# Kernel tuning notes

Hardware: AMD Instinct MI355X
Metric: run time of the kernel (lower is better)

The kernel has to match this reference:

```python
import jax, jax.numpy as jnp
import numpy as np

MAX_SEQ_LEN = 1000

def _ln(x, g, b, eps=1e-5):
    m = jnp.mean(x, -1, keepdims=True)
    v = jnp.var(x, -1, keepdims=True)
    return (x - m) * jax.lax.rsqrt(v + eps) * g + b

def _conv1d(x, k, b):
    # x [B,T,Cin], k [K,Cin,Cout], 'SAME' padding (odd kernel)
    return jax.lax.conv_general_dilated(x, k, (1,), 'SAME', dimension_numbers=('NWC', 'WIO', 'NWC')) + b

def _dwconv(x, w):
    # lightweight conv: softmax-normalized depthwise kernel, w [C,K]
    k = jnp.transpose(jax.nn.softmax(w, axis=1))[:, None, :]  # [K,1,C]
    return jax.lax.conv_general_dilated(x, k, (1,), 'SAME', dimension_numbers=('NWC', 'WIO', 'NWC'), feature_group_count=x.shape[-1])

def _conv2d(x, k, b):
    # x [B,H,W,Cin], k [kh,kw,Cin,Cout]
    return jax.lax.conv_general_dilated(x, k, (1, 1), 'SAME', dimension_numbers=('NHWC', 'HWIO', 'NHWC')) + b

def _lconv(x, mask, ln_g, ln_b, glu_w, glu_b, dw, out_w, out_b):
    # LConvBlock: LN -> GLU projection -> depthwise lightweight conv -> out proj -> residual, masked
    res = x
    h = _ln(x, ln_g, ln_b)
    h = h @ glu_w + glu_b
    a, g = jnp.split(h, 2, axis=-1)
    h = a * jax.nn.sigmoid(g)
    h = jnp.where(mask[..., None], 0.0, h)
    h = _dwconv(h, dw)
    h = h @ out_w + out_b
    h = h + res
    return jnp.where(mask[..., None], 0.0, h)

def _forward(content_embedding, speaker_embedding_B, rhythm_B, scaled_duration_outputs,
             in_w, in_b,
             lc0_ln_g, lc0_ln_b, lc0_glu_w, lc0_glu_b, lc0_dw, lc0_out_w, lc0_out_b,
             lc1_ln_g, lc1_ln_b, lc1_glu_w, lc1_glu_b, lc1_dw, lc1_out_w, lc1_out_b,
             p1_w, p1_b, p2_k, p2_b,
             cw_k, cw_b, cw_ln_g, cw_ln_b,
             mkb1_k, mkb1_b, mkb2_k, mkb2_b,
             lw_w, lw_b, ln_g, ln_b, text_mask):
    B, S, _ = content_embedding.shape
    spk = jnp.broadcast_to(speaker_embedding_B[:, None, :], (B, S, speaker_embedding_B.shape[-1]))
    x = jnp.concatenate([content_embedding, spk], -1) @ in_w + in_b
    # duration predictor
    V = _lconv(x, text_mask, lc0_ln_g, lc0_ln_b, lc0_glu_w, lc0_glu_b, lc0_dw, lc0_out_w, lc0_out_b)
    V = _lconv(V, text_mask, lc1_ln_g, lc1_ln_b, lc1_glu_w, lc1_glu_b, lc1_dw, lc1_out_w, lc1_out_b)
    D = jax.nn.softplus(V @ p1_w + p1_b)[..., 0]
    D = jnp.where(text_mask, 0.0, D)
    T = _conv1d(V, p2_k, p2_b)  # [B,S,upsampled_dim]
    # learnable upsampling
    pred_phoneme_len = scaled_duration_outputs.sum(-1)
    alpha_B = jax.lax.stop_gradient(pred_phoneme_len / rhythm_B) / D.sum(-1)
    sD = alpha_B[:, None] * D
    sV = alpha_B[:, None, None] * V
    sT = alpha_B[:, None, None] * T
    mel_len = jnp.clip(jnp.round(sD.sum(-1)).astype(jnp.int32), 1, MAX_SEQ_LEN)
    mel_mask = jnp.arange(MAX_SEQ_LEN)[None, :] >= mel_len[:, None]  # True = pad
    attn_mask = mel_mask[:, :, None] & text_mask[:, None, :]  # bmm(mel_mask, src_mask^T).bool()
    e_k = jnp.cumsum(sD, axis=1)
    s_k = e_k - sD
    t = jnp.arange(1, MAX_SEQ_LEN + 1, dtype=sD.dtype)[None, :, None]
    Sm = jnp.where(attn_mask, 0.0, t - s_k[:, None, :])
    Em = jnp.where(attn_mask, 0.0, e_k[:, None, :] - t)
    # conv_w block: conv1d -> relu -> LN
    Cv = _ln(jax.nn.relu(_conv1d(sV, cw_k, cw_b)), cw_ln_g, cw_ln_b)  # [B,S,CW]
    feat = jnp.concatenate([Sm[..., None], Em[..., None],
                            jnp.broadcast_to(Cv[:, None, :, :], (B, MAX_SEQ_LEN, S, Cv.shape[-1]))], -1)
    h = jax.nn.silu(_conv2d(feat, mkb1_k, mkb1_b))
    h = jax.nn.silu(_conv2d(h, mkb2_k, mkb2_b))
    Wsc = (h @ lw_w + lw_b)[..., 0]  # [B,mel,S]
    Wsc = jnp.where(attn_mask | text_mask[:, None, :], -jnp.inf, Wsc)
    Wmat = jax.nn.softmax(Wsc, axis=2)
    up = jnp.matmul(Wmat, sT)
    up = _ln(up, ln_g, ln_b)
    up = jnp.where(mel_mask[..., None], 0.0, up)
    return up, Wmat, alpha_B, mel_len, mel_mask

def setup_inputs() -> dict:
    key = jax.random.key(0)
    ks = iter(jax.random.split(key, 64))
    B, S, DC, DS, H, CW, MKB, K = 8, 256, 192, 64, 256, 16, 16, 3
    def w(shape, scale=0.02):
        return jax.random.normal(next(ks), shape, jnp.float32) * scale
    inp = {}
    inp['content_embedding'] = jax.random.normal(next(ks), (B, S, DC), jnp.float32)
    inp['speaker_embedding_B'] = jax.random.normal(next(ks), (B, DS), jnp.float32)
    inp['rhythm_B'] = 0.15 + 0.1 * jax.random.uniform(next(ks), (B,), jnp.float32)
    inp['scaled_duration_outputs'] = jax.random.uniform(next(ks), (B, S), jnp.float32)
    lens = jax.random.randint(next(ks), (B,), 200, S + 1)
    inp['text_mask'] = jnp.arange(S)[None, :] >= lens[:, None]
    inp['in_w'] = w((DC + DS, H)); inp['in_b'] = jnp.zeros((H,), jnp.float32)
    for i in range(2):
        inp[f'lc{i}_ln_g'] = jnp.ones((H,), jnp.float32); inp[f'lc{i}_ln_b'] = jnp.zeros((H,), jnp.float32)
        inp[f'lc{i}_glu_w'] = w((H, 2 * H)); inp[f'lc{i}_glu_b'] = jnp.zeros((2 * H,), jnp.float32)
        inp[f'lc{i}_dw'] = w((H, K), 1.0)
        inp[f'lc{i}_out_w'] = w((H, H)); inp[f'lc{i}_out_b'] = jnp.zeros((H,), jnp.float32)
    inp['p1_w'] = w((H, 1)); inp['p1_b'] = jnp.zeros((1,), jnp.float32)
    inp['p2_k'] = w((K, H, H)); inp['p2_b'] = jnp.zeros((H,), jnp.float32)
    inp['cw_k'] = w((K, H, CW)); inp['cw_b'] = jnp.zeros((CW,), jnp.float32)
    inp['cw_ln_g'] = jnp.ones((CW,), jnp.float32); inp['cw_ln_b'] = jnp.zeros((CW,), jnp.float32)
    inp['mkb1_k'] = w((K, K, CW + 2, MKB)); inp['mkb1_b'] = jnp.zeros((MKB,), jnp.float32)
    inp['mkb2_k'] = w((K, K, MKB, MKB)); inp['mkb2_b'] = jnp.zeros((MKB,), jnp.float32)
    inp['lw_w'] = w((MKB, 1)); inp['lw_b'] = jnp.zeros((1,), jnp.float32)
    inp['ln_g'] = jnp.ones((H,), jnp.float32); inp['ln_b'] = jnp.zeros((H,), jnp.float32)
    return inp

def reference(content_embedding, speaker_embedding_B, rhythm_B, scaled_duration_outputs,
              text_mask,
              in_w, in_b,
              lc0_ln_g, lc0_ln_b, lc0_glu_w, lc0_glu_b, lc0_dw, lc0_out_w, lc0_out_b,
              lc1_ln_g, lc1_ln_b, lc1_glu_w, lc1_glu_b, lc1_dw, lc1_out_w, lc1_out_b,
              p1_w, p1_b, p2_k, p2_b,
              cw_k, cw_b, cw_ln_g, cw_ln_b,
              mkb1_k, mkb1_b, mkb2_k, mkb2_b,
              lw_w, lw_b, ln_g, ln_b):
    return _forward(content_embedding, speaker_embedding_B, rhythm_B, scaled_duration_outputs,
                    in_w, in_b,
                    lc0_ln_g, lc0_ln_b, lc0_glu_w, lc0_glu_b, lc0_dw, lc0_out_w, lc0_out_b,
                    lc1_ln_g, lc1_ln_b, lc1_glu_w, lc1_glu_b, lc1_dw, lc1_out_w, lc1_out_b,
                    p1_w, p1_b, p2_k, p2_b,
                    cw_k, cw_b, cw_ln_g, cw_ln_b,
                    mkb1_k, mkb1_b, mkb2_k, mkb2_b,
                    lw_w, lw_b, ln_g, ln_b, text_mask)
```

## Files before the change

### kernel.cpp

```cpp
#include <hip/hip_runtime.h>
#include <math.h>

#define SS 256
#define HH 256
#define MLEN 1000
#define CWW 16
#define NOC 16
#define RB 24

typedef __attribute__((ext_vector_type(8))) short bfrag;
typedef __attribute__((ext_vector_type(4))) float ffrag;

#define WS_V2     1048576u
#define WS_STT    1835008u
#define WS_WB     2097152u
#define WS_CCV    2424832u
#define WS_SSV    2457600u
#define WS_CCI    2490368u
#define WS_SSI    2523136u
#define WS_CP     2555904u
#define WS_CV     2654208u
#define WS_EK     2686976u
#define WS_SK     2689024u
#define WS_ALPHA  2691072u
#define WS_MELI   2691080u
#define WS_TMASK  2691088u

#define PK_IN     0u
#define PK_GLU0   65536u
#define PK_GLU1   196608u
#define PK_OUT0   327680u
#define PK_OUT1   393216u
#define PK_P2     458752u

#define OUT_UP    0u
#define OUT_W     2048000u
#define OUT_ALPHA 4096000u
#define OUT_MLEN  4096008u
#define OUT_MMASK 4096016u

__device__ __forceinline__ unsigned bf16rne(float x){
  unsigned u=__float_as_uint(x);
  u += 0x7fffu + ((u>>16)&1u);
  return u;
}
__device__ __forceinline__ unsigned short bf16h(float x){ return (unsigned short)(bf16rne(x)>>16); }
__device__ __forceinline__ float bf2f(unsigned short u){ return __uint_as_float(((unsigned)u)<<16); }
__device__ __forceinline__ unsigned frag_idx(int k,int n,int KT){
  return (unsigned)(((((n>>4)*KT+(k>>5))*64 + ((k>>3)&3)*16 + (n&15))<<3) + (k&7));
}

__global__ __launch_bounds__(256) void k_prepmask(const void* __restrict__ traw,
    const float* __restrict__ in_w,
    const float* __restrict__ g0, const float* __restrict__ g1,
    const float* __restrict__ o0, const float* __restrict__ o1,
    const float* __restrict__ p2k, float* __restrict__ ws){
  int tid=threadIdx.x;
  if(blockIdx.x==256){
    __shared__ int s_fu, s_ff, s_nz;
    const unsigned char* mb=(const unsigned char*)traw;
    const unsigned int*  mw=(const unsigned int*)traw;
    if(tid==0){s_fu=0;s_ff=0;s_nz=0;}
    __syncthreads();
    int fu=0,ff=0,nz=0;
    for(int w=tid;w<512;w+=256){
      unsigned int v=mw[w];
      if(v){ nz=1; if(v==0x3F800000u) ff=1; else if(v&0xFFFFFF00u) fu=1; }
    }
    if(fu) atomicOr(&s_fu,1);
    if(ff) atomicOr(&s_ff,1);
    if(nz) atomicOr(&s_nz,1);
    __syncthreads();
    int words = (s_ff || (!s_fu && s_nz));
    for(int i=tid;i<2048;i+=256){
      unsigned int v = words ? mw[i] : (unsigned int)mb[i];
      ws[WS_TMASK+i] = v ? 1.0f : 0.0f;
    }
    return;
  }
  unsigned short* wb=(unsigned short*)(ws+WS_WB);
  int gid=blockIdx.x*256+tid, stride=65536;
  for(int i=gid;i<65536;i+=stride){ int k=i>>8,n=i&255; wb[PK_IN  +frag_idx(k,n,8)]=bf16h(in_w[i]); }
  for(int i=gid;i<131072;i+=stride){ int k=i>>9,n=i&511; wb[PK_GLU0+frag_idx(k,n,8)]=bf16h(g0[i]); }
  for(int i=gid;i<131072;i+=stride){ int k=i>>9,n=i&511; wb[PK_GLU1+frag_idx(k,n,8)]=bf16h(g1[i]); }
  for(int i=gid;i<65536;i+=stride){ int k=i>>8,n=i&255; wb[PK_OUT0+frag_idx(k,n,8)]=bf16h(o0[i]); }
  for(int i=gid;i<65536;i+=stride){ int k=i>>8,n=i&255; wb[PK_OUT1+frag_idx(k,n,8)]=bf16h(o1[i]); }
  for(int i=gid;i<196608;i+=stride){ int k3=i>>16,r=i&65535,k=r>>8,n=r&255;
    wb[PK_P2+(unsigned)k3*65536u+frag_idx(k,n,8)]=bf16h(p2k[i]); }
}

__global__ __launch_bounds__(256) void k_front(
    const float* __restrict__ ce, const float* __restrict__ spk,
    const unsigned short* __restrict__ wb, const float* __restrict__ in_b,
    const float* __restrict__ g0b, const float* __restrict__ ln0g, const float* __restrict__ ln0b,
    const float* __restrict__ dw0, const float* __restrict__ o0b,
    const float* __restrict__ g1b, const float* __restrict__ ln1g, const float* __restrict__ ln1b,
    const float* __restrict__ dw1, const float* __restrict__ o1b,
    const float* __restrict__ tmask, float* __restrict__ V2){
  __shared__ unsigned short Abf[16][264];
  __shared__ unsigned short Hb[16][264];
  __shared__ float Xf[16][264];
  __shared__ float Vf[16][264];
  __shared__ float dws[2][3][256];
  __shared__ float tmL[20];
  int b=blockIdx.x>>5, tile=blockIdx.x&31, s0=tile*8, tid=threadIdx.x;
  int w=tid>>6, lane=tid&63, lq=lane>>4, lm=lane&15;
  {
    float d0=dw0[tid*3],d1=dw0[tid*3+1],d2=dw0[tid*3+2];
    float mx=fmaxf(d0,fmaxf(d1,d2));
    float e0=__expf(d0-mx),e1=__expf(d1-mx),e2=__expf(d2-mx);
    float inv=1.0f/(e0+e1+e2);
    dws[0][0][tid]=e0*inv; dws[0][1][tid]=e1*inv; dws[0][2][tid]=e2*inv;
    d0=dw1[tid*3];d1=dw1[tid*3+1];d2=dw1[tid*3+2];
    mx=fmaxf(d0,fmaxf(d1,d2));
    e0=__expf(d0-mx);e1=__expf(d1-mx);e2=__expf(d2-mx);
    inv=1.0f/(e0+e1+e2);
    dws[1][0][tid]=e0*inv; dws[1][1][tid]=e1*inv; dws[1][2][tid]=e2*inv;
  }
  if(tid<18){
    int sI=s0-2+tid;
    tmL[tid]=(sI>=0&&sI<256)? tmask[b*256+sI] : 1.0f;
  }
  for(int it=0;it<16;it++){
    float v=0.f;
    int sI=s0-2+it;
    if(it<12 && sI>=0 && sI<256){
      int m=b*256+sI;
      v=(tid<192)? ce[m*192+tid] : spk[b*64+tid-192];
    }
    Abf[it][tid]=bf16h(v);
  }
  __syncthreads();
  {
    ffrag acc[4];
    #pragma unroll
    for(int j=0;j<4;j++){acc[j][0]=0;acc[j][1]=0;acc[j][2]=0;acc[j][3]=0;}
    #pragma unroll
    for(int kt=0;kt<8;kt++){
      bfrag af=*(const bfrag*)&Abf[lm][kt*32+lq*8];
      #pragma unroll
      for(int j=0;j<4;j++){
        int nt=w*4+j;
        bfrag bf=*(const bfrag*)(wb+PK_IN+((((unsigned)(nt*8+kt))*64u+(unsigned)lane)<<3));
        acc[j]=__builtin_amdgcn_mfma_f32_16x16x32_bf16(af,bf,acc[j],0,0,0);
      }
    }
    #pragma unroll
    for(int j=0;j<4;j++){
      int n=w*64+j*16+lm;
      float bn=in_b[n];
      #pragma unroll
      for(int reg=0;reg<4;reg++) Xf[lq*4+reg][n]=acc[j][reg]+bn;
    }
  }
  __syncthreads();
  {
    int r=tid>>4, seg=tid&15;
    if(r<12){
      float s=0.f,q=0.f;
      #pragma unroll
      for(int j4=0;j4<4;j4++){
        float4 v=*(const float4*)&Xf[r][seg*16+j4*4];
        s+=v.x+v.y+v.z+v.w; q+=v.x*v.x+v.y*v.y+v.z*v.z+v.w*v.w;
      }
      s+=__shfl_xor(s,1); q+=__shfl_xor(q,1);
      s+=__shfl_xor(s,2); q+=__shfl_xor(q,2);
      s+=__shfl_xor(s,4); q+=__shfl_xor(q,4);
      s+=__shfl_xor(s,8); q+=__shfl_xor(q,8);
      float mean=s*(1.0f/256.0f), rstd=rsqrtf(q*(1.0f/256.0f)-mean*mean+1e-5f);
      #pragma unroll
      for(int j4=0;j4<4;j4++){
        int c=seg*16+j4*4;
        float4 v=*(const float4*)&Xf[r][c];
        unsigned short q0=bf16h((v.x-mean)*rstd*ln0g[c+0]+ln0b[c+0]);
        unsigned short q1=bf16h((v.y-mean)*rstd*ln0g[c+1]+ln0b[c+1]);
        unsigned short q2=bf16h((v.z-mean)*rstd*ln0g[c+2]+ln0b[c+2]);
        unsigned short q3=bf16h((v.w-mean)*rstd*ln0g[c+3]+ln0b[c+3]);
        *(uint2*)&Abf[r][c]=make_uint2((unsigned)q0|((unsigned)q1<<16),(unsigned)q2|((unsigned)q3<<16));
      }
    } else {
      #pragma unroll
      for(int j4=0;j4<4;j4++) *(uint2*)&Abf[r][seg*16+j4*4]=make_uint2(0,0);
    }
  }
  __syncthreads();
  {
    ffrag aa[4],ag[4];
    #pragma unroll
    for(int j=0;j<4;j++){aa[j][0]=0;aa[j][1]=0;aa[j][2]=0;aa[j][3]=0;
                         ag[j][0]=0;ag[j][1]=0;ag[j][2]=0;ag[j][3]=0;}
    #pragma unroll
    for(int kt=0;kt<8;kt++){
      bfrag af=*(const bfrag*)&Abf[lm][kt*32+lq*8];
      #pragma unroll
      for(int j=0;j<4;j++){
        int nta=w*4+j, ntg=nta+16;
        bfrag bfa=*(const bfrag*)(wb+PK_GLU0+((((unsigned)(nta*8+kt))*64u+(unsigned)lane)<<3));
        bfrag bfg=*(const bfrag*)(wb+PK_GLU0+((((unsigned)(ntg*8+kt))*64u+(unsigned)lane)<<3));
        aa[j]=__builtin_amdgcn_mfma_f32_16x16x32_bf16(af,bfa,aa[j],0,0,0);
        ag[j]=__builtin_amdgcn_mfma_f32_16x16x32_bf16(af,bfg,ag[j],0,0,0);
      }
    }
    __syncthreads();
    #pragma unroll
    for(int j=0;j<4;j++){
      int n=w*64+j*16+lm;
      float ba=g0b[n], bg=g0b[n+256];
      #pragma unroll
      for(int reg=0;reg<4;reg++){
        int row=lq*4+reg;
        float a=aa[j][reg]+ba, g=ag[j][reg]+bg;
        float hv=a*(1.0f/(1.0f+__expf(-g)));
        if(row>=12||tmL[row]!=0.0f) hv=0.0f;
        Hb[row][n]=bf16h(hv);
      }
    }
  }
  __syncthreads();
  {
    float w0=dws[0][0][tid],w1=dws[0][1][tid],w2=dws[0][2][tid];
    for(int r=0;r<10;r++){
      float a=w0*bf2f(Hb[r][tid])+w1*bf2f(Hb[r+1][tid])+w2*bf2f(Hb[r+2][tid]);
      Abf[r][tid]=bf16h(a);
    }
    for(int r=10;r<16;r++) Abf[r][tid]=0;
  }
  __syncthreads();
  {
    ffrag acc[4];
    #pragma unroll
    for(int j=0;j<4;j++){acc[j][0]=0;acc[j][1]=0;acc[j][2]=0;acc[j][3]=0;}
    #pragma unroll
    for(int kt=0;kt<8;kt++){
      bfrag af=*(const bfrag*)&Abf[lm][kt*32+lq*8];
      #pragma unroll
      for(int j=0;j<4;j++){
        int nt=w*4+j;
        bfrag bf=*(const bfrag*)(wb+PK_OUT0+((((unsigned)(nt*8+kt))*64u+(unsigned)lane)<<3));
        acc[j]=__builtin_amdgcn_mfma_f32_16x16x32_bf16(af,bf,acc[j],0,0,0);
      }
    }
    #pragma unroll
    for(int j=0;j<4;j++){
      int n=w*64+j*16+lm;
      float bn=o0b[n];
      #pragma unroll
      for(int reg=0;reg<4;reg++){
        int row=lq*4+reg;
        float v=(row<10 && tmL[row+1]==0.0f)? acc[j][reg]+bn+Xf[row+1][n] : 0.0f;
        Vf[row][n]=v;
      }
    }
  }
  __syncthreads();
  {
    int r=tid>>4, seg=tid&15;
    if(r<10){
      float s=0.f,q=0.f;
      #pragma unroll
      for(int j4=0;j4<4;j4++){
        float4 v=*(const float4*)&Vf[r][seg*16+j4*4];
        s+=v.x+v.y+v.z+v.w; q+=v.x*v.x+v.y*v.y+v.z*v.z+v.w*v.w;
      }
      s+=__shfl_xor(s,1); q+=__shfl_xor(q,1);
      s+=__shfl_xor(s,2); q+=__shfl_xor(q,2);
      s+=__shfl_xor(s,4); q+=__shfl_xor(q,4);
      s+=__shfl_xor(s,8); q+=__shfl_xor(q,8);
      float mean=s*(1.0f/256.0f), rstd=rsqrtf(q*(1.0f/256.0f)-mean*mean+1e-5f);
      #pragma unroll
      for(int j4=0;j4<4;j4++){
        int c=seg*16+j4*4;
        float4 v=*(const float4*)&Vf[r][c];
        unsigned short q0=bf16h((v.x-mean)*rstd*ln1g[c+0]+ln1b[c+0]);
        unsigned short q1=bf16h((v.y-mean)*rstd*ln1g[c+1]+ln1b[c+1]);
        unsigned short q2=bf16h((v.z-mean)*rstd*ln1g[c+2]+ln1b[c+2]);
        unsigned short q3=bf16h((v.w-mean)*rstd*ln1g[c+3]+ln1b[c+3]);
        *(uint2*)&Abf[r][c]=make_uint2((unsigned)q0|((unsigned)q1<<16),(unsigned)q2|((unsigned)q3<<16));
      }
    } else {
      #pragma unroll
      for(int j4=0;j4<4;j4++) *(uint2*)&Abf[r][seg*16+j4*4]=make_uint2(0,0);
    }
  }
  __syncthreads();
  {
    ffrag aa[4],ag[4];
    #pragma unroll
    for(int j=0;j<4;j++){aa[j][0]=0;aa[j][1]=0;aa[j][2]=0;aa[j][3]=0;
                         ag[j][0]=0;ag[j][1]=0;ag[j][2]=0;ag[j][3]=0;}
    #pragma unroll
    for(int kt=0;kt<8;kt++){
      bfrag af=*(const bfrag*)&Abf[lm][kt*32+lq*8];
      #pragma unroll
      for(int j=0;j<4;j++){
        int nta=w*4+j, ntg=nta+16;
        bfrag bfa=*(const bfrag*)(wb+PK_GLU1+((((unsigned)(nta*8+kt))*64u+(unsigned)lane)<<3));
        bfrag bfg=*(const bfrag*)(wb+PK_GLU1+((((unsigned)(ntg*8+kt))*64u+(unsigned)lane)<<3));
        aa[j]=__builtin_amdgcn_mfma_f32_16x16x32_bf16(af,bfa,aa[j],0,0,0);
        ag[j]=__builtin_amdgcn_mfma_f32_16x16x32_bf16(af,bfg,ag[j],0,0,0);
      }
    }
    __syncthreads();
    #pragma unroll
    for(int j=0;j<4;j++){
      int n=w*64+j*16+lm;
      float ba=g1b[n], bg=g1b[n+256];
      #pragma unroll
      for(int reg=0;reg<4;reg++){
        int row=lq*4+reg;
        float a=aa[j][reg]+ba, g=ag[j][reg]+bg;
        float hv=a*(1.0f/(1.0f+__expf(-g)));
        if(row>=10||tmL[row+1]!=0.0f) hv=0.0f;
        Hb[row][n]=bf16h(hv);
      }
    }
  }
  __syncthreads();
  {
    float w0=dws[1][0][tid],w1=dws[1][1][tid],w2=dws[1][2][tid];
    for(int r=0;r<8;r++){
      float a=w0*bf2f(Hb[r][tid])+w1*bf2f(Hb[r+1][tid])+w2*bf2f(Hb[r+2][tid]);
      Abf[r][tid]=bf16h(a);
    }
    for(int r=8;r<16;r++) Abf[r][tid]=0;
  }
  __syncthreads();
  {
    ffrag acc[4];
    #pragma unroll
    for(int j=0;j<4;j++){acc[j][0]=0;acc[j][1]=0;acc[j][2]=0;acc[j][3]=0;}
    #pragma unroll
    for(int kt=0;kt<8;kt++){
      bfrag af=*(const bfrag*)&Abf[lm][kt*32+lq*8];
      #pragma unroll
      for(int j=0;j<4;j++){
        int nt=w*4+j;
        bfrag bf=*(const bfrag*)(wb+PK_OUT1+((((unsigned)(nt*8+kt))*64u+(unsigned)lane)<<3));
        acc[j]=__builtin_amdgcn_mfma_f32_16x16x32_bf16(af,bf,acc[j],0,0,0);
      }
    }
    #pragma unroll
    for(int j=0;j<4;j++){
      int n=w*64+j*16+lm;
      float bn=o1b[n];
      #pragma unroll
      for(int reg=0;reg<4;reg++){
        int row=lq*4+reg;
        if(row<8){
          float v=(tmL[row+2]!=0.0f)? 0.0f : acc[j][reg]+bn+Vf[row+1][n];
          V2[(unsigned)(b*256+s0+row)*256u+n]=v;
        }
      }
    }
  }
}

__global__ __launch_bounds__(256) void k_dur(const float* __restrict__ V2, const float* __restrict__ p1w,
    const float* __restrict__ p1b, const float* __restrict__ sdo, const float* __restrict__ rhythm,
    float* __restrict__ ws, float* __restrict__ outp){
  __shared__ float p1[HH];
  __shared__ float sd[SS];
  __shared__ float red[16];
  int b=blockIdx.x, tid=threadIdx.x;
  int wid=tid>>6, lane=tid&63;
  p1[tid]=p1w[tid];
  __syncthreads();
  float accd=p1b[0];
  const float* row=V2+(unsigned)(b*SS+tid)*HH;
  for(int k=0;k<HH;k+=4){
    float4 v=*(const float4*)&row[k];
    accd+=v.x*p1[k]+v.y*p1[k+1]+v.z*p1[k+2]+v.w*p1[k+3];
  }
  float Dv=fmaxf(accd,0.0f)+log1pf(expf(-fabsf(accd)));
  if(ws[WS_TMASK+b*SS+tid]!=0.0f) Dv=0.0f;
  float sv=sdo[b*SS+tid];
  float a=Dv, c=sv;
  for(int off=32;off;off>>=1){ a+=__shfl_down(a,off); c+=__shfl_down(c,off); }
  if(lane==0){ red[wid]=a; red[wid+8]=c; }
  __syncthreads();
  float Dsum=red[0]+red[1]+red[2]+red[3];
  float pred=red[8]+red[9]+red[10]+red[11];
  float al=(pred/rhythm[b])/Dsum;
  float sDv=al*Dv;
  sd[tid]=sDv;
  __syncthreads();
  for(int off=1;off<SS;off<<=1){
    float t=(tid>=off)?sd[tid-off]:0.0f;
    __syncthreads();
    sd[tid]+=t;
    __syncthreads();
  }
  float ek=sd[tid], sk=ek-sDv;
  ws[WS_EK+b*SS+tid]=ek;
  ws[WS_SK+b*SS+tid]=sk;
  float melf=sd[SS-1];
  int mel=(int)rintf(melf); mel=mel<1?1:(mel>MLEN?MLEN:mel);
  if(tid==0){
    ws[WS_ALPHA+b]=al;
    ((int*)ws)[WS_MELI+b]=mel;
    outp[OUT_ALPHA+b]=al;
    outp[OUT_MLEN+b]=(float)mel;
  }
  for(int t=tid;t<MLEN;t+=SS) outp[OUT_MMASK+b*MLEN+t]=(t>=mel)?1.0f:0.0f;
}

__global__ __launch_bounds__(256) void k_post(const float* __restrict__ V2,
    const unsigned short* __restrict__ wbp2, const float* __restrict__ p2b,
    const float* __restrict__ cwk, const float* __restrict__ cwb,
    const float* __restrict__ cwg, const float* __restrict__ cwbe,
    const float* __restrict__ mkb1k, const float* __restrict__ mkb1b,
    float* __restrict__ ws){
  int bx=blockIdx.x, tid=threadIdx.x;
  if(bx<256){
    __shared__ unsigned short Abf[18][264];
    int m0=(bx>>1)*16, nh=bx&1, b=m0>>8, s0=m0&255;
    for(int it=0;it<18;it++){
      int sI=s0-1+it;
      float v=(sI>=0&&sI<256)? V2[(unsigned)(b*256+sI)*256u+tid] : 0.0f;
      Abf[it][tid]=bf16h(v);
    }
    __syncthreads();
    int w=tid>>6, lane=tid&63, lq=lane>>4, lm=lane&15;
    ffrag acc[2];
    #pragma unroll
    for(int tt=0;tt<2;tt++){ acc[tt][0]=0;acc[tt][1]=0;acc[tt][2]=0;acc[tt][3]=0; }
    for(int k3=0;k3<3;k3++){
      const unsigned short* wb3=wbp2+(unsigned)k3*65536u;
      #pragma unroll
      for(int kt=0;kt<8;kt++){
        bfrag af=*(const bfrag*)&Abf[lm+k3][kt*32+lq*8];
        #pragma unroll
        for(int tt=0;tt<2;tt++){
          int nt=nh*8+w*2+tt;
          bfrag bf=*(const bfrag*)(wb3+((((unsigned)(nt*8+kt))*64u+(unsigned)lane)<<3));
          acc[tt]=__builtin_amdgcn_mfma_f32_16x16x32_bf16(af,bf,acc[tt],0,0,0);
        }
      }
    }
    float al=ws[WS_ALPHA+b];
    unsigned short* stt=(unsigned short*)(ws+WS_STT);
    #pragma unroll
    for(int tt=0;tt<2;tt++){
      int n=nh*128+w*32+tt*16+lm;
      float bn=p2b[n];
      unsigned short o0=bf16h((acc[tt][0]+bn)*al);
      unsigned short o1=bf16h((acc[tt][1]+bn)*al);
      unsigned short o2=bf16h((acc[tt][2]+bn)*al);
      unsigned short o3=bf16h((acc[tt][3]+bn)*al);
      *(uint2*)&stt[((unsigned)(b*256+n)<<8)+(unsigned)(s0+lq*4)]=
        make_uint2((unsigned)o0|((unsigned)o1<<16),(unsigned)o2|((unsigned)o3<<16));
    }
  } else if(bx<384){
    __shared__ float Vt[18][SS];
    int bb=bx-256;
    int b=bb>>4, tile=bb&15;
    int sbase=tile*16;
    float al=ws[WS_ALPHA+b];
    for(int rr=0;rr<18;rr++){
      int s=sbase-1+rr;
      Vt[rr][tid]=(s>=0&&s<SS)?al*V2[(b*SS+s)*HH+tid]:0.0f;
    }
    __syncthreads();
    int sl=tid>>4, oc=tid&15;
    float a0=cwb[oc],a1=0.f,a2=0.f,a3=0.f;
    for(int k3=0;k3<3;k3++){
      const float* vp=&Vt[sl+k3][0];
      const float* wpp=cwk+(unsigned)k3*HH*CWW+oc;
      for(int c=0;c<HH;c+=4){
        a0+=vp[c+0]*wpp[(c+0)*CWW];
        a1+=vp[c+1]*wpp[(c+1)*CWW];
        a2+=vp[c+2]*wpp[(c+2)*CWW];
        a3+=vp[c+3]*wpp[(c+3)*CWW];
      }
    }
    float acc=fmaxf((a0+a1)+(a2+a3),0.0f);
    float ssum=acc, qsum=acc*acc;
    for(int off=8;off;off>>=1){ ssum+=__shfl_xor(ssum,off); qsum+=__shfl_xor(qsum,off); }
    float mean=ssum*(1.0f/CWW), var=qsum*(1.0f/CWW)-mean*mean;
    float cv=(acc-mean)*rsqrtf(var+1e-5f)*cwg[oc]+cwbe[oc];
    ws[WS_CV+(unsigned)(b*SS+sbase+sl)*CWW+oc]=cv;
  } else {
    __shared__ float CvL[258][17];
    __shared__ float k1c[3][3][CWW][NOC];
    __shared__ float kab[3][3][2][NOC];
    __shared__ float skE[258], ekE[258], fiE[258];
    int b=bx-384;
    for(int i=tid;i<3*3*CWW*NOC;i+=256){
      int oc=i&15, ic=(i>>4)&15, kk=i>>8;
      int kw=kk%3, kh=kk/3;
      k1c[kh][kw][ic][oc]=mkb1k[((kh*3+kw)*18+2+ic)*NOC+oc];
    }
    for(int i=tid;i<3*3*2*NOC;i+=256){
      int oc=i&15, ch=(i>>4)&1, kk=i>>5;
      int kw=kk%3, kh=kk/3;
      kab[kh][kw][ch][oc]=mkb1k[((kh*3+kw)*18+ch)*NOC+oc];
    }
    for(int i=tid;i<SS*CWW;i+=256) CvL[1+(i>>4)][i&15]=ws[WS_CV+(unsigned)b*SS*CWW+i];
    if(tid<CWW){ CvL[0][tid]=0.f; CvL[257][tid]=0.f; }
    if(tid<258){
      float sk=0.f, ek=0.f, fi=0.f;
      if(tid>=1 && tid<=SS){
        sk=ws[WS_SK+b*SS+tid-1];
        ek=ws[WS_EK+b*SS+tid-1];
        fi=(ws[WS_TMASK+b*SS+tid-1]!=0.0f)?0.0f:1.0f;
      }
      skE[tid]=sk; ekE[tid]=ek; fiE[tid]=fi;
    }
    __syncthreads();
    float* cpg=ws+WS_CP+(unsigned)b*3*SS*NOC;
    float ccv[16],ssv[16],cci[16],ssi[16];
    #pragma unroll
    for(int oc=0;oc<NOC;oc++){ float bb2=mkb1b[oc]; ccv[oc]=bb2; cci[oc]=bb2; ssv[oc]=0.f; ssi[oc]=0.f; }
    for(int dt=0;dt<3;dt++){
      float acc[NOC];
      #pragma unroll
      for(int oc=0;oc<NOC;oc++) acc[oc]=0.f;
      #pragma unroll
      for(int ds=0;ds<3;ds++){
        #pragma unroll
        for(int ic=0;ic<CWW;ic++){
          float v=CvL[tid+ds][ic];
          #pragma unroll
          for(int oc=0;oc<NOC;oc++) acc[oc]+=v*k1c[dt][ds][ic][oc];
        }
      }
      for(int oc=0;oc<NOC;oc++) cpg[(unsigned)(dt*SS+tid)*NOC+oc]=acc[oc];
      float va[16],vb[16],ia[16],ib2[16];
      #pragma unroll
      for(int oc=0;oc<NOC;oc++){ va[oc]=0.f; vb[oc]=0.f; ia[oc]=0.f; ib2[oc]=0.f; }
      #pragma unroll
      for(int ds=0;ds<3;ds++){
        int j=tid+ds;
        float inb=(j>=1&&j<=SS)?1.0f:0.0f;
        float fb=fiE[j];
        float skv=skE[j], ekv=ekE[j];
        #pragma unroll
        for(int oc=0;oc<NOC;oc++){
          float ka=kab[dt][ds][0][oc], kb=kab[dt][ds][1][oc];
          float d=ka-kb, e=kb*ekv-ka*skv;
          va[oc]+=inb*d; vb[oc]+=inb*e; ia[oc]+=fb*d; ib2[oc]+=fb*e;
        }
      }
      float dtf=(float)dt;
      #pragma unroll
      for(int oc=0;oc<NOC;oc++){
        ccv[oc]+=acc[oc]+vb[oc]+dtf*va[oc]; ssv[oc]+=va[oc];
        cci[oc]+=acc[oc]+ib2[oc]+dtf*ia[oc]; ssi[oc]+=ia[oc];
      }
    }
    unsigned base=(unsigned)(b*SS+tid)*16u;
    for(int oc=0;oc<NOC;oc++){
      ws[WS_CCV+base+oc]=ccv[oc];
      ws[WS_SSV+base+oc]=ssv[oc];
      ws[WS_CCI+base+oc]=cci[oc];
      ws[WS_SSI+base+oc]=ssi[oc];
    }
  }
}

__global__ __launch_bounds__(256,4) void k_stageB(
    const float* __restrict__ ws, const float* __restrict__ mkb1k, const float* __restrict__ mkb1b,
    const float* __restrict__ mkb2k, const float* __restrict__ mkb2b,
    const float* __restrict__ lww, const float* __restrict__ lwb,
    float* __restrict__ outp){
  __shared__ short ringh[3][258][RB];
  __shared__ float skL[258], ekL[258];
  __shared__ unsigned char finC[260];
  __shared__ __align__(16) float wscL[SS];
  __shared__ float red[16];
  int bx=blockIdx.x, b=bx/125, chunk=bx%125, t0=chunk*8, tid=threadIdx.x;
  int wid=tid>>6, lane=tid&63;
  int lq=lane>>4, lm=lane&15;
  if(tid<258){
    float sk=0.f, ek=0.f; unsigned char fin=0;
    if(tid>=1 && tid<=SS){
      sk=ws[WS_SK+b*SS+tid-1];
      ek=ws[WS_EK+b*SS+tid-1];
      fin=(ws[WS_TMASK+b*SS+tid-1]!=0.0f)?0:1;
    }
    skL[tid]=sk; ekL[tid]=ek; finC[tid]=fin;
  }
  if(tid<72){
    int sl=tid/24, rem=tid%24;
    int row=(rem<12)?0:257, c=(rem%12)*2;
    *(int*)&ringh[sl][row][c]=0;
  }
  int mel=((const int*)ws)[WS_MELI+b];
  __syncthreads();

  const float* cpb=ws+WS_CP+(unsigned)b*3*SS*NOC;

  unsigned offA[5]; int dtL[5], zgL[5];
  bfrag bfw[5];
  {
    #pragma unroll
    for(int i=0;i<5;i++){
      int g=4*i+lq;
      int dt,ds,hf,zg;
      if(g<18){ dt=g/6; int rm=g-6*dt; ds=rm>>1; hf=rm&1; zg=0; }
      else { dt=0; ds=0; hf=0; zg=1; }
      int srow=wid*64+lm+ds;
      offA[i]=(unsigned)((srow*RB+8*hf)*2);
      dtL[i]=dt; zgL[i]=zg;
      int pk[4];
      if(!zg){
        #pragma unroll
        for(int j=0;j<4;j++){
          unsigned u0=bf16rne(mkb2k[(8*g+2*j)*NOC+lm]);
          unsigned u1=bf16rne(mkb2k[(8*g+2*j+1)*NOC+lm]);
          pk[j]=(int)((u0>>16)|(u1&0xffff0000u));
        }
      } else pk[0]=pk[1]=pk[2]=pk[3]=0;
      bfw[i]=__builtin_bit_cast(bfrag, make_int4(pk[0],pk[1],pk[2],pk[3]));
    }
  }
  float b2v=mkb2b[lm];
  float lwwv=lww[lm];
  float lwb0=lwb[0];
  const char* ringB=(const char*)&ringh[0][0][0];
  bfrag azero={};

  auto conv1row=[&](int T){
    int s=tid;
    float acc[NOC];
    bool fv=(T>=1)&&(T<=998)&&(T+1<mel);
    bool fi=(T>=2)&&(T<=998)&&(T-1>=mel);
    if(fv||fi){
      const float* cc=ws+(fv?WS_CCV:WS_CCI)+(unsigned)(b*SS+s)*16u;
      const float* s2=ws+(fv?WS_SSV:WS_SSI)+(unsigned)(b*SS+s)*16u;
      float Tf=(float)T;
      #pragma unroll
      for(int q=0;q<4;q++){
        float4 c4=((const float4*)cc)[q];
        float4 s4=((const float4*)s2)[q];
        acc[4*q+0]=c4.x+Tf*s4.x; acc[4*q+1]=c4.y+Tf*s4.y;
        acc[4*q+2]=c4.z+Tf*s4.z; acc[4*q+3]=c4.w+Tf*s4.w;
      }
    } else {
      #pragma unroll
      for(int oc=0;oc<NOC;oc++) acc[oc]=mkb1b[oc];
      #pragma unroll
      for(int dt=0;dt<3;dt++){
        int tr=T+dt-1;
        if(tr<0||tr>=MLEN) continue;
        bool valid=(tr<mel);
        float tt=(float)(tr+1);
        float gg[3], hh[3];
        #pragma unroll
        for(int ds=0;ds<3;ds++){
          int j=s+ds;
          float f = valid ? ((j>=1&&j<=SS)?1.0f:0.0f) : (float)finC[j];
          gg[ds]=f*(tt-skL[j]);
          hh[ds]=f*(ekL[j]-tt);
        }
        const float* cpr=cpb+(unsigned)(dt*SS+s)*NOC;
        float4 c0=((const float4*)cpr)[0], c1=((const float4*)cpr)[1];
        float4 c2=((const float4*)cpr)[2], c3=((const float4*)cpr)[3];
        acc[0]+=c0.x; acc[1]+=c0.y; acc[2]+=c0.z; acc[3]+=c0.w;
        acc[4]+=c1.x; acc[5]+=c1.y; acc[6]+=c1.z; acc[7]+=c1.w;
        acc[8]+=c2.x; acc[9]+=c2.y; acc[10]+=c2.z; acc[11]+=c2.w;
        acc[12]+=c3.x; acc[13]+=c3.y; acc[14]+=c3.z; acc[15]+=c3.w;
        #pragma unroll
        for(int ds=0;ds<3;ds++){
          const float* kA=mkb1k+((dt*3+ds)*18+0)*NOC;
          const float* kB=mkb1k+((dt*3+ds)*18+1)*NOC;
          #pragma unroll
          for(int oc=0;oc<NOC;oc++) acc[oc]+=gg[ds]*kA[oc]+hh[ds]*kB[oc];
        }
      }
    }
    int slot=T%3;
    int pk[8];
    #pragma unroll
    for(int j=0;j<8;j++){
      float x0=acc[2*j], x1=acc[2*j+1];
      float s0=x0/(1.0f+__expf(-x0));
      float s1=x1/(1.0f+__expf(-x1));
      unsigned u0=bf16rne(s0), u1=bf16rne(s1);
      pk[j]=(int)((u0>>16)|(u1&0xffff0000u));
    }
    int4* dst=(int4*)&ringh[slot][s+1][0];
    dst[0]=make_int4(pk[0],pk[1],pk[2],pk[3]);
    dst[1]=make_int4(pk[4],pk[5],pk[6],pk[7]);
  };

  if(t0>0) conv1row(t0-1);
  conv1row(t0);

  #pragma unroll 1
  for(int r=0;r<8;r++){
    int t=t0+r;
    if(t+1<MLEN) conv1row(t+1);
    __syncthreads();
    int tmod=t%3;
    ffrag acc2[4];
    #pragma unroll
    for(int tt=0;tt<4;tt++){ acc2[tt][0]=b2v; acc2[tt][1]=b2v; acc2[tt][2]=b2v; acc2[tt][3]=b2v; }
    #pragma unroll
    for(int i=0;i<5;i++){
      int dt=dtL[i];
      int x=tmod+dt+2; x=(x>=3)?x-3:x; x=(x>=3)?x-3:x;
      int tr=t+dt-1;
      bool av=((unsigned)tr<(unsigned)MLEN)&&(!zgL[i]);
      const char* rp=ringB+(unsigned)x*(258u*RB*2u)+offA[i];
      #pragma unroll
      for(int tt=0;tt<4;tt++){
        int4 ra=*(const int4*)(rp+tt*(16*RB*2));
        bfrag a=av?__builtin_bit_cast(bfrag,ra):azero;
        acc2[tt]=__builtin_amdgcn_mfma_f32_16x16x32_bf16(a,bfw[i],acc2[tt],0,0,0);
      }
    }
    #pragma unroll
    for(int tt=0;tt<4;tt++){
      float out4[4];
      #pragma unroll
      for(int q=0;q<4;q++){
        float xx=acc2[tt][q];
        float pv=(xx/(1.0f+__expf(-xx)))*lwwv;
        pv+=__shfl_xor(pv,1); pv+=__shfl_xor(pv,2); pv+=__shfl_xor(pv,4); pv+=__shfl_xor(pv,8);
        out4[q]=pv+lwb0;
      }
      if(lm==0){
        *(float4*)&wscL[wid*64+tt*16+lq*4]=make_float4(out4[0],out4[1],out4[2],out4[3]);
      }
    }
    __syncthreads();
    float fm=(float)finC[tid+1];
    float wsc=wscL[tid];
    float val=(fm!=0.0f)?wsc:-3.0e38f;
    float mx=val;
    for(int off=32;off;off>>=1) mx=fmaxf(mx,__shfl_down(mx,off));
    if(lane==0) red[wid]=mx;
    __syncthreads();
    mx=fmaxf(fmaxf(red[0],red[1]),fmaxf(red[2],red[3]));
    float e=(fm!=0.0f)?__expf(wsc-mx):0.0f;
    float sm=e;
    for(int off=32;off;off>>=1) sm+=__shfl_down(sm,off);
    if(lane==0) red[8+wid]=sm;
    __syncthreads();
    sm=red[8]+red[9]+red[10]+red[11];
    outp[OUT_W+(unsigned)(b*MLEN+t)*SS+tid]=e/sm;
    __syncthreads();
  }
}

__global__ __launch_bounds__(256) void k_up(const float* __restrict__ ws,
    const float* __restrict__ lng, const float* __restrict__ lnb, float* __restrict__ outp){
  __shared__ unsigned short Wbf[16][264];
  __shared__ float UpL[16][264];
  __shared__ float gb[2][256];
  int bx=blockIdx.x, b=bx/63, tile=bx%63, t0=tile*16, tid=threadIdx.x;
  gb[0][tid]=lng[tid]; gb[1][tid]=lnb[tid];
  for(int it=0;it<16;it++){
    int t=t0+it;
    float v=(t<MLEN)? outp[OUT_W+(unsigned)(b*MLEN+t)*256u+tid] : 0.0f;
    Wbf[it][tid]=bf16h(v);
  }
  int mel=((const int*)ws)[WS_MELI+b];
  __syncthreads();
  int w=tid>>6, lane=tid&63, lq=lane>>4, lm=lane&15;
  const unsigned short* stt=(const unsigned short*)(ws+WS_STT)+(unsigned)b*65536u;
  ffrag acc[4];
  #pragma unroll
  for(int tt=0;tt<4;tt++){ acc[tt][0]=0;acc[tt][1]=0;acc[tt][2]=0;acc[tt][3]=0; }
  #pragma unroll
  for(int kt=0;kt<8;kt++){
    bfrag af=*(const bfrag*)&Wbf[lm][kt*32+lq*8];
    #pragma unroll
    for(int tt=0;tt<4;tt++){
      int n=w*64+tt*16+lm;
      bfrag bf=*(const bfrag*)(stt+((unsigned)n<<8)+(unsigned)(kt*32+lq*8));
      acc[tt]=__builtin_amdgcn_mfma_f32_16x16x32_bf16(af,bf,acc[tt],0,0,0);
    }
  }
  #pragma unroll
  for(int tt=0;tt<4;tt++){
    #pragma unroll
    for(int reg=0;reg<4;reg++)
      UpL[lq*4+reg][w*64+tt*16+lm]=acc[tt][reg];
  }
  __syncthreads();
  int r=tid>>4, seg=tid&15;
  float s=0.f,q=0.f;
  #pragma unroll
  for(int j4=0;j4<4;j4++){
    float4 v=*(const float4*)&UpL[r][seg*16+j4*4];
    s+=v.x+v.y+v.z+v.w; q+=v.x*v.x+v.y*v.y+v.z*v.z+v.w*v.w;
  }
  s+=__shfl_xor(s,1); q+=__shfl_xor(q,1);
  s+=__shfl_xor(s,2); q+=__shfl_xor(q,2);
  s+=__shfl_xor(s,4); q+=__shfl_xor(q,4);
  s+=__shfl_xor(s,8); q+=__shfl_xor(q,8);
  float mean=s*(1.0f/256.0f), rstd=rsqrtf(q*(1.0f/256.0f)-mean*mean+1e-5f);
  int t=t0+r;
  if(t<MLEN){
    bool vld=(t<mel);
    #pragma unroll
    for(int j4=0;j4<4;j4++){
      int c=seg*16+j4*4;
      float4 v=*(const float4*)&UpL[r][c];
      float4 o;
      o.x=vld?((v.x-mean)*rstd*gb[0][c+0]+gb[1][c+0]):0.0f;
      o.y=vld?((v.y-mean)*rstd*gb[0][c+1]+gb[1][c+1]):0.0f;
      o.z=vld?((v.z-mean)*rstd*gb[0][c+2]+gb[1][c+2]):0.0f;
      o.w=vld?((v.w-mean)*rstd*gb[0][c+3]+gb[1][c+3]):0.0f;
      *(float4*)&outp[OUT_UP+(unsigned)(b*MLEN+t)*256u+c]=o;
    }
  }
}

extern "C" void kernel_launch(void* const* d_in, const int* in_sizes, int n_in,
                              void* d_out, int out_size, void* d_ws, size_t ws_size,
                              hipStream_t stream){
  const float* ce   =(const float*)d_in[0];
  const float* spk  =(const float*)d_in[1];
  const float* rhy  =(const float*)d_in[2];
  const float* sdo  =(const float*)d_in[3];
  const void*  tmr  =d_in[4];
  const float* in_w =(const float*)d_in[5];
  const float* in_b =(const float*)d_in[6];
  const float* l0lg =(const float*)d_in[7];
  const float* l0lb =(const float*)d_in[8];
  const float* l0gw =(const float*)d_in[9];
  const float* l0gb =(const float*)d_in[10];
  const float* l0dw =(const float*)d_in[11];
  const float* l0ow =(const float*)d_in[12];
  const float* l0ob =(const float*)d_in[13];
  const float* l1lg =(const float*)d_in[14];
  const float* l1lb =(const float*)d_in[15];
  const float* l1gw =(const float*)d_in[16];
  const float* l1gb =(const float*)d_in[17];
  const float* l1dw =(const float*)d_in[18];
  const float* l1ow =(const float*)d_in[19];
  const float* l1ob =(const float*)d_in[20];
  const float* p1w  =(const float*)d_in[21];
  const float* p1b  =(const float*)d_in[22];
  const float* p2k  =(const float*)d_in[23];
  const float* p2b  =(const float*)d_in[24];
  const float* cwk  =(const float*)d_in[25];
  const float* cwb  =(const float*)d_in[26];
  const float* cwg  =(const float*)d_in[27];
  const float* cwbe =(const float*)d_in[28];
  const float* m1k  =(const float*)d_in[29];
  const float* m1b  =(const float*)d_in[30];
  const float* m2k  =(const float*)d_in[31];
  const float* m2b  =(const float*)d_in[32];
  const float* lww  =(const float*)d_in[33];
  const float* lwbp =(const float*)d_in[34];
  const float* lng  =(const float*)d_in[35];
  const float* lnb  =(const float*)d_in[36];
  float* ws=(float*)d_ws;
  float* outp=(float*)d_out;
  const unsigned short* wbb=(const unsigned short*)(ws+WS_WB);

  k_prepmask<<<257,256,0,stream>>>(tmr, in_w, l0gw, l1gw, l0ow, l1ow, p2k, ws);
  k_front   <<<256,256,0,stream>>>(ce, spk, wbb, in_b,
                                   l0gb, l0lg, l0lb, l0dw, l0ob,
                                   l1gb, l1lg, l1lb, l1dw, l1ob,
                                   ws+WS_TMASK, ws+WS_V2);
  k_dur     <<<8,256,0,stream>>>(ws+WS_V2, p1w, p1b, sdo, rhy, ws, outp);
  k_post    <<<392,256,0,stream>>>(ws+WS_V2, wbb+PK_P2, p2b, cwk, cwb, cwg, cwbe, m1k, m1b, ws);
  k_stageB  <<<1000,256,0,stream>>>(ws, m1k, m1b, m2k, m2b, lww, lwbp, outp);
  k_up      <<<504,256,0,stream>>>(ws, lng, lnb, outp);
}
```

Baseline: 310.6 us.

## Halve k_front row tile to double block count; split cp stage into own kernel

k_front now handles 4 output rows per block instead of 8 and launches 512 blocks instead of 256. The goal is better fill of the GPU's compute units for this short front-end chain. The cost is more redundant halo rows per output, and the 16-row MFMA tiles are now mostly padding. The cp/mkb1 precompute branch moves out of k_post into its own 8-block kernel, which runs after the conv-LN blocks that write WS_CV. This removes the same-launch dependency but adds one more kernel launch.

```diff
diff --git a/kernel.cpp b/kernel.cpp
--- a/kernel.cpp
+++ b/kernel.cpp
@@ -98,12 +98,12 @@
     const float* __restrict__ dw1, const float* __restrict__ o1b,
     const float* __restrict__ tmask, float* __restrict__ V2){
   __shared__ unsigned short Abf[16][264];
-  __shared__ unsigned short Hb[16][264];
-  __shared__ float Xf[16][264];
-  __shared__ float Vf[16][264];
+  __shared__ unsigned short Hb[8][264];
+  __shared__ float Xf[8][264];
+  __shared__ float Vf[8][264];
   __shared__ float dws[2][3][256];
-  __shared__ float tmL[20];
-  int b=blockIdx.x>>5, tile=blockIdx.x&31, s0=tile*8, tid=threadIdx.x;
+  __shared__ float tmL[8];
+  int b=blockIdx.x>>6, tile=blockIdx.x&63, s0=tile*4, tid=threadIdx.x;
   int w=tid>>6, lane=tid&63, lq=lane>>4, lm=lane&15;
   {
     float d0=dw0[tid*3],d1=dw0[tid*3+1],d2=dw0[tid*3+2];
@@ -117,19 +117,20 @@
     inv=1.0f/(e0+e1+e2);
     dws[1][0][tid]=e0*inv; dws[1][1][tid]=e1*inv; dws[1][2][tid]=e2*inv;
   }
-  if(tid<18){
+  if(tid<8){
     int sI=s0-2+tid;
     tmL[tid]=(sI>=0&&sI<256)? tmask[b*256+sI] : 1.0f;
   }
-  for(int it=0;it<16;it++){
+  for(int it=0;it<8;it++){
     float v=0.f;
     int sI=s0-2+it;
-    if(it<12 && sI>=0 && sI<256){
+    if(sI>=0 && sI<256){
       int m=b*256+sI;
       v=(tid<192)? ce[m*192+tid] : spk[b*64+tid-192];
     }
     Abf[it][tid]=bf16h(v);
   }
+  for(int it=8;it<16;it++) Abf[it][tid]=0;
   __syncthreads();
   {
     ffrag acc[4];
@@ -150,13 +151,16 @@
       int n=w*64+j*16+lm;
       float bn=in_b[n];
       #pragma unroll
-      for(int reg=0;reg<4;reg++) Xf[lq*4+reg][n]=acc[j][reg]+bn;
+      for(int reg=0;reg<4;reg++){
+        int row=lq*4+reg;
+        if(row<8) Xf[row][n]=acc[j][reg]+bn;
+      }
     }
   }
   __syncthreads();
   {
     int r=tid>>4, seg=tid&15;
-    if(r<12){
+    if(r<8){
       float s=0.f,q=0.f;
       #pragma unroll
       for(int j4=0;j4<4;j4++){
@@ -178,9 +182,6 @@
         unsigned short q3=bf16h((v.w-mean)*rstd*ln0g[c+3]+ln0b[c+3]);
         *(uint2*)&Abf[r][c]=make_uint2((unsigned)q0|((unsigned)q1<<16),(unsigned)q2|((unsigned)q3<<16));
       }
-    } else {
-      #pragma unroll
-      for(int j4=0;j4<4;j4++) *(uint2*)&Abf[r][seg*16+j4*4]=make_uint2(0,0);
     }
   }
   __syncthreads();
@@ -209,21 +210,23 @@
       #pragma unroll
       for(int reg=0;reg<4;reg++){
         int row=lq*4+reg;
-        float a=aa[j][reg]+ba, g=ag[j][reg]+bg;
-        float hv=a*(1.0f/(1.0f+__expf(-g)));
-        if(row>=12||tmL[row]!=0.0f) hv=0.0f;
-        Hb[row][n]=bf16h(hv);
+        if(row<8){
+          float a=aa[j][reg]+ba, g=ag[j][reg]+bg;
+          float hv=a*(1.0f/(1.0f+__expf(-g)));
+          if(tmL[row]!=0.0f) hv=0.0f;
+          Hb[row][n]=bf16h(hv);
+        }
       }
     }
   }
   __syncthreads();
   {
     float w0=dws[0][0][tid],w1=dws[0][1][tid],w2=dws[0][2][tid];
-    for(int r=0;r<10;r++){
+    for(int r=0;r<6;r++){
       float a=w0*bf2f(Hb[r][tid])+w1*bf2f(Hb[r+1][tid])+w2*bf2f(Hb[r+2][tid]);
       Abf[r][tid]=bf16h(a);
     }
-    for(int r=10;r<16;r++) Abf[r][tid]=0;
+    Abf[6][tid]=0; Abf[7][tid]=0;
   }
   __syncthreads();
   {
@@ -247,15 +250,17 @@
       #pragma unroll
       for(int reg=0;reg<4;reg++){
         int row=lq*4+reg;
-        float v=(row<10 && tmL[row+1]==0.0f)? acc[j][reg]+bn+Xf[row+1][n] : 0.0f;
-        Vf[row][n]=v;
+        if(row<6){
+          float v=(tmL[row+1]==0.0f)? acc[j][reg]+bn+Xf[row+1][n] : 0.0f;
+          Vf[row][n]=v;
+        }
       }
     }
   }
   __syncthreads();
   {
     int r=tid>>4, seg=tid&15;
-    if(r<10){
+    if(r<6){
       float s=0.f,q=0.f;
       #pragma unroll
       for(int j4=0;j4<4;j4++){
@@ -277,9 +282,6 @@
         unsigned short q3=bf16h((v.w-mean)*rstd*ln1g[c+3]+ln1b[c+3]);
         *(uint2*)&Abf[r][c]=make_uint2((unsigned)q0|((unsigned)q1<<16),(unsigned)q2|((unsigned)q3<<16));
       }
-    } else {
-      #pragma unroll
-      for(int j4=0;j4<4;j4++) *(uint2*)&Abf[r][seg*16+j4*4]=make_uint2(0,0);
     }
   }
   __syncthreads();
@@ -308,21 +310,23 @@
       #pragma unroll
       for(int reg=0;reg<4;reg++){
         int row=lq*4+reg;
-        float a=aa[j][reg]+ba, g=ag[j][reg]+bg;
-        float hv=a*(1.0f/(1.0f+__expf(-g)));
-        if(row>=10||tmL[row+1]!=0.0f) hv=0.0f;
-        Hb[row][n]=bf16h(hv);
+        if(row<6){
+          float a=aa[j][reg]+ba, g=ag[j][reg]+bg;
+          float hv=a*(1.0f/(1.0f+__expf(-g)));
+          if(tmL[row+1]!=0.0f) hv=0.0f;
+          Hb[row][n]=bf16h(hv);
+        }
       }
     }
   }
   __syncthreads();
   {
     float w0=dws[1][0][tid],w1=dws[1][1][tid],w2=dws[1][2][tid];
-    for(int r=0;r<8;r++){
+    for(int r=0;r<4;r++){
       float a=w0*bf2f(Hb[r][tid])+w1*bf2f(Hb[r+1][tid])+w2*bf2f(Hb[r+2][tid]);
       Abf[r][tid]=bf16h(a);
     }
-    for(int r=8;r<16;r++) Abf[r][tid]=0;
+    Abf[4][tid]=0; Abf[5][tid]=0;
   }
   __syncthreads();
   {
@@ -346,7 +350,7 @@
       #pragma unroll
       for(int reg=0;reg<4;reg++){
         int row=lq*4+reg;
-        if(row<8){
+        if(row<4){
           float v=(tmL[row+2]!=0.0f)? 0.0f : acc[j][reg]+bn+Vf[row+1][n];
           V2[(unsigned)(b*256+s0+row)*256u+n]=v;
         }
@@ -408,7 +412,6 @@
     const unsigned short* __restrict__ wbp2, const float* __restrict__ p2b,
     const float* __restrict__ cwk, const float* __restrict__ cwb,
     const float* __restrict__ cwg, const float* __restrict__ cwbe,
-    const float* __restrict__ mkb1k, const float* __restrict__ mkb1b,
     float* __restrict__ ws){
   int bx=blockIdx.x, tid=threadIdx.x;
   if(bx<256){
@@ -450,7 +453,7 @@
       *(uint2*)&stt[((unsigned)(b*256+n)<<8)+(unsigned)(s0+lq*4)]=
         make_uint2((unsigned)o0|((unsigned)o1<<16),(unsigned)o2|((unsigned)o3<<16));
     }
-  } else if(bx<384){
+  } else {
     __shared__ float Vt[18][SS];
     int bb=bx-256;
     int b=bb>>4, tile=bb&15;
@@ -479,82 +482,85 @@
     float mean=ssum*(1.0f/CWW), var=qsum*(1.0f/CWW)-mean*mean;
     float cv=(acc-mean)*rsqrtf(var+1e-5f)*cwg[oc]+cwbe[oc];
     ws[WS_CV+(unsigned)(b*SS+sbase+sl)*CWW+oc]=cv;
-  } else {
-    __shared__ float CvL[258][17];
-    __shared__ float k1c[3][3][CWW][NOC];
-    __shared__ float kab[3][3][2][NOC];
-    __shared__ float skE[258], ekE[258], fiE[258];
-    int b=bx-384;
-    for(int i=tid;i<3*3*CWW*NOC;i+=256){
-      int oc=i&15, ic=(i>>4)&15, kk=i>>8;
-      int kw=kk%3, kh=kk/3;
-      k1c[kh][kw][ic][oc]=mkb1k[((kh*3+kw)*18+2+ic)*NOC+oc];
-    }
-    for(int i=tid;i<3*3*2*NOC;i+=256){
-      int oc=i&15, ch=(i>>4)&1, kk=i>>5;
-      int kw=kk%3, kh=kk/3;
-      kab[kh][kw][ch][oc]=mkb1k[((kh*3+kw)*18+ch)*NOC+oc];
-    }
-    for(int i=tid;i<SS*CWW;i+=256) CvL[1+(i>>4)][i&15]=ws[WS_CV+(unsigned)b*SS*CWW+i];
-    if(tid<CWW){ CvL[0][tid]=0.f; CvL[257][tid]=0.f; }
-    if(tid<258){
-      float sk=0.f, ek=0.f, fi=0.f;
-      if(tid>=1 && tid<=SS){
-        sk=ws[WS_SK+b*SS+tid-1];
-        ek=ws[WS_EK+b*SS+tid-1];
-        fi=(ws[WS_TMASK+b*SS+tid-1]!=0.0f)?0.0f:1.0f;
-      }
-      skE[tid]=sk; ekE[tid]=ek; fiE[tid]=fi;
-    }
-    __syncthreads();
-    float* cpg=ws+WS_CP+(unsigned)b*3*SS*NOC;
-    float ccv[16],ssv[16],cci[16],ssi[16];
-    #pragma unroll
-    for(int oc=0;oc<NOC;oc++){ float bb2=mkb1b[oc]; ccv[oc]=bb2; cci[oc]=bb2; ssv[oc]=0.f; ssi[oc]=0.f; }
-    for(int dt=0;dt<3;dt++){
-      float acc[NOC];
-      #pragma unroll
-      for(int oc=0;oc<NOC;oc++) acc[oc]=0.f;
-      #pragma unroll
-      for(int ds=0;ds<3;ds++){
+  }
+}
+
+__global__ __launch_bounds__(256) void k_cp(const float* __restrict__ mkb1k, const float* __restrict__ mkb1b,
+    float* __restrict__ ws){
+  __shared__ float CvL[258][17];
+  __shared__ float k1c[3][3][CWW][NOC];
+  __shared__ float kab[3][3][2][NOC];
+  __shared__ float skE[258], ekE[258], fiE[258];
+  int b=blockIdx.x, tid=threadIdx.x;
+  for(int i=tid;i<3*3*CWW*NOC;i+=256){
+    int oc=i&15, ic=(i>>4)&15, kk=i>>8;
+    int kw=kk%3, kh=kk/3;
+    k1c[kh][kw][ic][oc]=mkb1k[((kh*3+kw)*18+2+ic)*NOC+oc];
+  }
+  for(int i=tid;i<3*3*2*NOC;i+=256){
+    int oc=i&15, ch=(i>>4)&1, kk=i>>5;
+    int kw=kk%3, kh=kk/3;
+    kab[kh][kw][ch][oc]=mkb1k[((kh*3+kw)*18+ch)*NOC+oc];
+  }
+  for(int i=tid;i<SS*CWW;i+=256) CvL[1+(i>>4)][i&15]=ws[WS_CV+(unsigned)b*SS*CWW+i];
+  if(tid<CWW){ CvL[0][tid]=0.f; CvL[257][tid]=0.f; }
+  if(tid<258){
+    float sk=0.f, ek=0.f, fi=0.f;
+    if(tid>=1 && tid<=SS){
+      sk=ws[WS_SK+b*SS+tid-1];
+      ek=ws[WS_EK+b*SS+tid-1];
+      fi=(ws[WS_TMASK+b*SS+tid-1]!=0.0f)?0.0f:1.0f;
+    }
+    skE[tid]=sk; ekE[tid]=ek; fiE[tid]=fi;
+  }
+  __syncthreads();
+  float* cpg=ws+WS_CP+(unsigned)b*3*SS*NOC;
+  float ccv[16],ssv[16],cci[16],ssi[16];
+  #pragma unroll
+  for(int oc=0;oc<NOC;oc++){ float bb2=mkb1b[oc]; ccv[oc]=bb2; cci[oc]=bb2; ssv[oc]=0.f; ssi[oc]=0.f; }
+  for(int dt=0;dt<3;dt++){
+    float acc[NOC];
+    #pragma unroll
+    for(int oc=0;oc<NOC;oc++) acc[oc]=0.f;
+    #pragma unroll
+    for(int ds=0;ds<3;ds++){
+      #pragma unroll
+      for(int ic=0;ic<CWW;ic++){
+        float v=CvL[tid+ds][ic];
         #pragma unroll
-        for(int ic=0;ic<CWW;ic++){
-          float v=CvL[tid+ds][ic];
-          #pragma unroll
-          for(int oc=0;oc<NOC;oc++) acc[oc]+=v*k1c[dt][ds][ic][oc];
-        }
-      }
-      for(int oc=0;oc<NOC;oc++) cpg[(unsigned)(dt*SS+tid)*NOC+oc]=acc[oc];
-      float va[16],vb[16],ia[16],ib2[16];
-      #pragma unroll
-      for(int oc=0;oc<NOC;oc++){ va[oc]=0.f; vb[oc]=0.f; ia[oc]=0.f; ib2[oc]=0.f; }
-      #pragma unroll
-      for(int ds=0;ds<3;ds++){
-        int j=tid+ds;
-        float inb=(j>=1&&j<=SS)?1.0f:0.0f;
-        float fb=fiE[j];
-        float skv=skE[j], ekv=ekE[j];
-        #pragma unroll
-        for(int oc=0;oc<NOC;oc++){
-          float ka=kab[dt][ds][0][oc], kb=kab[dt][ds][1][oc];
-          float d=ka-kb, e=kb*ekv-ka*skv;
-          va[oc]+=inb*d; vb[oc]+=inb*e; ia[oc]+=fb*d; ib2[oc]+=fb*e;
-        }
-      }
-      float dtf=(float)dt;
+        for(int oc=0;oc<NOC;oc++) acc[oc]+=v*k1c[dt][ds][ic][oc];
+      }
+    }
+    for(int oc=0;oc<NOC;oc++) cpg[(unsigned)(dt*SS+tid)*NOC+oc]=acc[oc];
+    float va[16],vb[16],ia[16],ib2[16];
+    #pragma unroll
+    for(int oc=0;oc<NOC;oc++){ va[oc]=0.f; vb[oc]=0.f; ia[oc]=0.f; ib2[oc]=0.f; }
+    #pragma unroll
+    for(int ds=0;ds<3;ds++){
+      int j=tid+ds;
+      float inb=(j>=1&&j<=SS)?1.0f:0.0f;
+      float fb=fiE[j];
+      float skv=skE[j], ekv=ekE[j];
       #pragma unroll
       for(int oc=0;oc<NOC;oc++){
-        ccv[oc]+=acc[oc]+vb[oc]+dtf*va[oc]; ssv[oc]+=va[oc];
-        cci[oc]+=acc[oc]+ib2[oc]+dtf*ia[oc]; ssi[oc]+=ia[oc];
-      }
-    }
-    unsigned base=(unsigned)(b*SS+tid)*16u;
+        float ka=kab[dt][ds][0][oc], kb=kab[dt][ds][1][oc];
+        float d=ka-kb, e=kb*ekv-ka*skv;
+        va[oc]+=inb*d; vb[oc]+=inb*e; ia[oc]+=fb*d; ib2[oc]+=fb*e;
+      }
+    }
+    float dtf=(float)dt;
+    #pragma unroll
     for(int oc=0;oc<NOC;oc++){
-      ws[WS_CCV+base+oc]=ccv[oc];
-      ws[WS_SSV+base+oc]=ssv[oc];
-      ws[WS_CCI+base+oc]=cci[oc];
-      ws[WS_SSI+base+oc]=ssi[oc];
-    }
+      ccv[oc]+=acc[oc]+vb[oc]+dtf*va[oc]; ssv[oc]+=va[oc];
+      cci[oc]+=acc[oc]+ib2[oc]+dtf*ia[oc]; ssi[oc]+=ia[oc];
+    }
+  }
+  unsigned base=(unsigned)(b*SS+tid)*16u;
+  for(int oc=0;oc<NOC;oc++){
+    ws[WS_CCV+base+oc]=ccv[oc];
+    ws[WS_SSV+base+oc]=ssv[oc];
+    ws[WS_CCI+base+oc]=cci[oc];
+    ws[WS_SSI+base+oc]=ssi[oc];
   }
 }
 
@@ -854,12 +860,13 @@
   const unsigned short* wbb=(const unsigned short*)(ws+WS_WB);
 
   k_prepmask<<<257,256,0,stream>>>(tmr, in_w, l0gw, l1gw, l0ow, l1ow, p2k, ws);
-  k_front   <<<256,256,0,stream>>>(ce, spk, wbb, in_b,
+  k_front   <<<512,256,0,stream>>>(ce, spk, wbb, in_b,
                                    l0gb, l0lg, l0lb, l0dw, l0ob,
                                    l1gb, l1lg, l1lb, l1dw, l1ob,
                                    ws+WS_TMASK, ws+WS_V2);
   k_dur     <<<8,256,0,stream>>>(ws+WS_V2, p1w, p1b, sdo, rhy, ws, outp);
-  k_post    <<<392,256,0,stream>>>(ws+WS_V2, wbb+PK_P2, p2b, cwk, cwb, cwg, cwbe, m1k, m1b, ws);
+  k_post    <<<384,256,0,stream>>>(ws+WS_V2, wbb+PK_P2, p2b, cwk, cwb, cwg, cwbe, ws);
+  k_cp      <<<8,256,0,stream>>>(m1k, m1b, ws);
   k_stageB  <<<1000,256,0,stream>>>(ws, m1k, m1b, m2k, m2b, lww, lwbp, outp);
   k_up      <<<504,256,0,stream>>>(ws, lng, lnb, outp);
 }
```

Result: slower. 324.5 us (+4.5%).
